# Optimization experiments

Measured on AMD Instinct MI355X. Metric: run time of the kernel, lower is better.

The kernel has to match this reference:

```python
import jax, jax.numpy as jnp
import numpy as np

NEG_SLOPE = 0.2  # PyG GATConv default leaky_relu slope


def gat_conv(x, src, dst, n, W, a_src, a_dst, bias, concat):
    """PyG-style GATConv (add_self_loops already applied to src/dst)."""
    H, C = a_src.shape
    h = (x @ W).reshape(n, H, C)                      # [N,H,C]
    al_src = jnp.einsum('nhc,hc->nh', h, a_src)       # [N,H]
    al_dst = jnp.einsum('nhc,hc->nh', h, a_dst)       # [N,H]
    e = jax.nn.leaky_relu(al_src[src] + al_dst[dst], NEG_SLOPE)  # [E,H]
    # segment softmax over incoming edges of each dst node
    m = jax.ops.segment_max(e, dst, num_segments=n)   # [N,H]
    ex = jnp.exp(e - m[dst])
    denom = jax.ops.segment_sum(ex, dst, num_segments=n)
    alpha = ex / denom[dst]                            # [E,H]
    out = jax.ops.segment_sum(h[src] * alpha[:, :, None], dst, num_segments=n)  # [N,H,C]
    if concat:
        out = out.reshape(n, H * C)
    else:
        out = out.mean(axis=1)
    return out + bias


def setup_inputs() -> dict:
    key = jax.random.key(0)
    ks = jax.random.split(key, 12)
    N, E = 100000, 1600000
    IN, HID, OUT, H = 128, 16, 32, 4
    x = jax.random.normal(ks[0], (N, IN), dtype=jnp.float32)
    edge_index = jax.random.randint(ks[1], (2, E), 0, N, dtype=jnp.int64)
    s = 0.1
    W1 = jax.random.normal(ks[2], (IN, H * HID), dtype=jnp.float32) * s
    a_src1 = jax.random.normal(ks[3], (H, HID), dtype=jnp.float32) * s
    a_dst1 = jax.random.normal(ks[4], (H, HID), dtype=jnp.float32) * s
    b1 = jnp.zeros((H * HID,), dtype=jnp.float32)
    W2 = jax.random.normal(ks[5], (H * HID, H * OUT), dtype=jnp.float32) * s
    a_src2 = jax.random.normal(ks[6], (H, OUT), dtype=jnp.float32) * s
    a_dst2 = jax.random.normal(ks[7], (H, OUT), dtype=jnp.float32) * s
    b2 = jnp.zeros((OUT,), dtype=jnp.float32)
    return {"x": x, "edge_index": edge_index,
            "W1": W1, "a_src1": a_src1, "a_dst1": a_dst1, "b1": b1,
            "W2": W2, "a_src2": a_src2, "a_dst2": a_dst2, "b2": b2}


def reference(x, edge_index, W1, a_src1, a_dst1, b1, W2, a_src2, a_dst2, b2):
    n = x.shape[0]
    loop = jnp.arange(n, dtype=edge_index.dtype)
    src = jnp.concatenate([edge_index[0], loop])
    dst = jnp.concatenate([edge_index[1], loop])
    # dropout is identity at inference
    h = gat_conv(x, src, dst, n, W1, a_src1, a_dst1, b1, concat=True)
    h = gat_conv(h, src, dst, n, W2, a_src2, a_dst2, b2, concat=False)
    h = jax.nn.elu(h)
    return jax.nn.log_softmax(h, axis=1)
```

## Files before the change

### kernel.cpp

```cpp
#include <hip/hip_runtime.h>
#include <hip/hip_fp16.h>
#include <cstdint>
#include <cstddef>

#define NEG 0.2f
#define TILE 4096
#define WEXP(e) __expf((e) > 0.f ? (e) : NEG * (e))

typedef int i4v __attribute__((ext_vector_type(4)));

__device__ __forceinline__ i4v ld_i4(const int* p) {
    i4v r;
    __builtin_memcpy(&r, p, 16);
    return r;
}
__device__ __forceinline__ __half2 bch(unsigned v) { __half2 r; *(unsigned*)&r = v; return r; }
__device__ __forceinline__ __half2 bchi(int v) { __half2 r; *(int*)&r = v; return r; }


__global__ __launch_bounds__(256) void bhist_k(const int* __restrict__ ei, int* __restrict__ bc, int E, int nbk) {
    __shared__ int sb[256];
    int t = threadIdx.x;
    sb[t] = 0;
    __syncthreads();
    int stride = gridDim.x * 256;
    for (int i = blockIdx.x * 256 + t; i < E; i += stride) {
        int d = __builtin_nontemporal_load(ei + E + i);
        atomicAdd(&sb[d >> 9], 1);
    }
    __syncthreads();
    if (t < nbk && sb[t] > 0) atomicAdd(&bc[t], sb[t]);
}


__global__ __launch_bounds__(256) void bscan_k(const int* __restrict__ bc, int* __restrict__ bb,
                                               int* __restrict__ curA, int nbk) {
    __shared__ int sm[256];
    int t = threadIdx.x;
    int v = (t < nbk) ? bc[t] : 0;
    sm[t] = v; __syncthreads();
    for (int off = 1; off < 256; off <<= 1) {
        int u = (t >= off) ? sm[t - off] : 0;
        __syncthreads();
        sm[t] += u;
        __syncthreads();
    }
    if (t < nbk) {
        int ex = sm[t] - v;
        bb[t] = ex;
        curA[t] = ex;
        if (t == nbk - 1) bb[nbk] = sm[t];
    }
}


__global__ __launch_bounds__(256) void partA_k(const int* __restrict__ ei, int* __restrict__ curA,
                                               uint2* __restrict__ pairs, int E, int nbk) {
    __shared__ int scnt[256];
    __shared__ int sc[256];
    __shared__ int sbase[256];
    __shared__ int gbase[256];
    __shared__ int cur2[256];
    __shared__ int ssrc[TILE];
    __shared__ int sdst[TILE];
    int t = threadIdx.x;
    int ntiles = (E + TILE - 1) / TILE;
    for (int tile = blockIdx.x; tile < ntiles; tile += gridDim.x) {
        int base = tile * TILE;
        int cntE = min(TILE, E - base);
        scnt[t] = 0;
        __syncthreads();
        int mys[16], myd[16];
        #pragma unroll
        for (int j = 0; j < 16; j++) {
            int i = base + t + 256 * j;
            int s = 0, d = -1;
            if (i < E) {
                s = __builtin_nontemporal_load(ei + i);
                d = __builtin_nontemporal_load(ei + E + i);
            }
            mys[j] = s; myd[j] = d;
            if (d >= 0) atomicAdd(&scnt[d >> 9], 1);
        }
        __syncthreads();
        sc[t] = scnt[t];
        __syncthreads();
        for (int off = 1; off < 256; off <<= 1) {
            int u = (t >= off) ? sc[t - off] : 0;
            __syncthreads();
            sc[t] += u;
            __syncthreads();
        }
        int myb = sc[t] - scnt[t];
        sbase[t] = myb;
        cur2[t] = myb;
        if (t < nbk && scnt[t] > 0) gbase[t] = atomicAdd(&curA[t], scnt[t]);
        __syncthreads();
        #pragma unroll
        for (int j = 0; j < 16; j++) {
            int d = myd[j];
            if (d >= 0) {
                int b = d >> 9;
                int pos = atomicAdd(&cur2[b], 1);
                ssrc[pos] = mys[j];
                sdst[pos] = d;
            }
        }
        __syncthreads();
        for (int i = t; i < cntE; i += 256) {
            int d = sdst[i];
            int b = d >> 9;
            int addr = gbase[b] + (i - sbase[b]);
            pairs[addr] = make_uint2((unsigned)ssrc[i], (unsigned)d);
        }
        __syncthreads();
    }
}


__global__ __launch_bounds__(256) void partB2_k(const uint2* __restrict__ pin, const int* __restrict__ bb,
                                                int* __restrict__ rp, int* __restrict__ cnt,
                                                int* __restrict__ srcout, int N) {
    __shared__ int cur[512];
    __shared__ int sc[512];
    int b = blockIdx.x, t = threadIdx.x;
    int d0 = b << 9;
    cur[t] = 0; cur[t + 256] = 0;
    __syncthreads();
    int ebase = bb[b], eend = bb[b + 1];
    for (int j = ebase + t; j < eend; j += 256) {
        int d = (int)pin[j].y;
        atomicAdd(&cur[d - d0], 1);
    }
    __syncthreads();
    sc[t] = cur[t]; sc[t + 256] = cur[t + 256];
    __syncthreads();
    for (int off = 1; off <= 256; off <<= 1) {
        int a0 = (t >= off) ? sc[t - off] : 0;
        int a1 = sc[t + 256 - off];
        __syncthreads();
        sc[t] += a0; sc[t + 256] += a1;
        __syncthreads();
    }
    int base0 = ebase + sc[t] - cur[t];
    int base1 = ebase + sc[t + 256] - cur[t + 256];
    if (d0 + t < N)       { rp[d0 + t] = base0;       cnt[d0 + t] = cur[t]; }
    if (d0 + t + 256 < N) { rp[d0 + t + 256] = base1; cnt[d0 + t + 256] = cur[t + 256]; }
    cur[t] = base0; cur[t + 256] = base1;
    __syncthreads();
    for (int j = ebase + t; j < eend; j += 256) {
        uint2 p = pin[j];
        int d = (int)p.y;
        int pos = rp[d] + 0;
        pos = atomicAdd(&cur[d - d0], 1);
        srcout[pos] = (int)p.x;
    }
}


__global__ __launch_bounds__(256) void gemm1_k(const float* __restrict__ x, const float* __restrict__ W,
                                               const float* __restrict__ a_src, const float* __restrict__ a_dst,
                                               __half* __restrict__ h, float* __restrict__ alsrc,
                                               float* __restrict__ aldst, int N) {
    __shared__ float Bs[128 * 64];
    __shared__ float xt[64 * 68];
    int t = threadIdx.x;
    for (int i = t; i < 128 * 64 / 4; i += 256)
        ((float4*)Bs)[i] = ((const float4*)W)[i];
    int ct = t & 15, rt = t >> 4;
    int head = ct >> 2, cq = ct & 3;
    float asv[4], adv[4];
    #pragma unroll
    for (int j = 0; j < 4; j++) {
        asv[j] = a_src[head * 16 + 4 * cq + j];
        adv[j] = a_dst[head * 16 + 4 * cq + j];
    }
    int ntiles = (N + 63) >> 6;
    for (int tile = blockIdx.x; tile < ntiles; tile += gridDim.x) {
        int r0 = tile << 6;
        float acc[4][4];
        #pragma unroll
        for (int i = 0; i < 4; i++)
            #pragma unroll
            for (int j = 0; j < 4; j++) acc[i][j] = 0.f;
        for (int kc = 0; kc < 128; kc += 64) {
            __syncthreads();
            int srow = t >> 4, sf4 = t & 15;
            #pragma unroll
            for (int p = 0; p < 4; p++) {
                int r = r0 + srow + 16 * p;
                float4 v = make_float4(0.f, 0.f, 0.f, 0.f);
                if (r < N) v = *(const float4*)(x + (size_t)r * 128 + kc + 4 * sf4);
                int rr = srow + 16 * p, k0 = 4 * sf4;
                int colb = 4 * (((rr >> 2) + sf4) & 15) + (rr & 3);
                xt[(k0 + 0) * 68 + colb] = v.x;
                xt[(k0 + 1) * 68 + colb] = v.y;
                xt[(k0 + 2) * 68 + colb] = v.z;
                xt[(k0 + 3) * 68 + colb] = v.w;
            }
            __syncthreads();
            #pragma unroll 4
            for (int k = 0; k < 64; k++) {
                float4 bv = *(float4*)&Bs[(kc + k) * 64 + 4 * ct];
                float4 xv = *(float4*)&xt[k * 68 + 4 * ((rt + (k >> 2)) & 15)];
                acc[0][0] = fmaf(xv.x, bv.x, acc[0][0]);
                acc[0][1] = fmaf(xv.x, bv.y, acc[0][1]);
                acc[0][2] = fmaf(xv.x, bv.z, acc[0][2]);
                acc[0][3] = fmaf(xv.x, bv.w, acc[0][3]);
                acc[1][0] = fmaf(xv.y, bv.x, acc[1][0]);
                acc[1][1] = fmaf(xv.y, bv.y, acc[1][1]);
                acc[1][2] = fmaf(xv.y, bv.z, acc[1][2]);
                acc[1][3] = fmaf(xv.y, bv.w, acc[1][3]);
                acc[2][0] = fmaf(xv.z, bv.x, acc[2][0]);
                acc[2][1] = fmaf(xv.z, bv.y, acc[2][1]);
                acc[2][2] = fmaf(xv.z, bv.z, acc[2][2]);
                acc[2][3] = fmaf(xv.z, bv.w, acc[2][3]);
                acc[3][0] = fmaf(xv.w, bv.x, acc[3][0]);
                acc[3][1] = fmaf(xv.w, bv.y, acc[3][1]);
                acc[3][2] = fmaf(xv.w, bv.z, acc[3][2]);
                acc[3][3] = fmaf(xv.w, bv.w, acc[3][3]);
            }
        }
        #pragma unroll
        for (int i = 0; i < 4; i++) {
            int r = r0 + 4 * rt + i;
            float ps = 0.f, pd = 0.f;
            #pragma unroll
            for (int j = 0; j < 4; j++) {
                ps = fmaf(acc[i][j], asv[j], ps);
                pd = fmaf(acc[i][j], adv[j], pd);
            }
            ps += __shfl_xor(ps, 1); ps += __shfl_xor(ps, 2);
            pd += __shfl_xor(pd, 1); pd += __shfl_xor(pd, 2);
            if (r < N) {
                __half2 h0 = __floats2half2_rn(acc[i][0], acc[i][1]);
                __half2 h1 = __floats2half2_rn(acc[i][2], acc[i][3]);
                *(__half2*)(h + (size_t)r * 64 + 4 * ct) = h0;
                *(__half2*)(h + (size_t)r * 64 + 4 * ct + 2) = h1;
                if (cq == 0) { alsrc[r * 4 + head] = ps; aldst[r * 4 + head] = pd; }
            }
        }
    }
}


__global__ __launch_bounds__(256) void prew_k(const float* __restrict__ W2, const float* __restrict__ as2,
                                              const float* __restrict__ ad2, float* __restrict__ was,
                                              float* __restrict__ wad, unsigned* __restrict__ wkh) {
    int t = threadIdx.x;
    int k = t >> 2, hh = t & 3;
    const float* wrow = W2 + k * 128 + hh * 32;
    const float* av = as2 + hh * 32;
    const float* dv = ad2 + hh * 32;
    float s = 0.f, ds = 0.f;
    #pragma unroll 8
    for (int c = 0; c < 32; c++) {
        float w = wrow[c];
        s = fmaf(w, av[c], s);
        ds = fmaf(w, dv[c], ds);
    }
    was[t] = s;
    wad[t] = ds;
    #pragma unroll
    for (int j = 0; j < 16; j++) {
        int e = t * 16 + j;
        int r = e >> 6, cc = e & 63;
        int col = cc >> 1, par = cc & 1;
        int p = 2 * r + par;
        int h = p >> 5, kk = (2 * p) & 63;
        float f0 = W2[kk * 128 + h * 32 + col];
        float f1 = W2[(kk + 1) * 128 + h * 32 + col];
        __half2 hv = __floats2half2_rn(f0, f1);
        wkh[e] = *(unsigned*)&hv;
    }
}


__global__ __launch_bounds__(256) void node1_k(const __half* __restrict__ h, const int* __restrict__ srccol,
                                               const float* __restrict__ alsrc, const float* __restrict__ aldst,
                                               const int* __restrict__ rp, const int* __restrict__ cnt,
                                               const float* __restrict__ bias,
                                               const float* __restrict__ was, const float* __restrict__ wad,
                                               __half* __restrict__ out,
                                               float* __restrict__ alsrc2, float* __restrict__ aldst2, int N) {
    int t = threadIdx.x;
    int d = (blockIdx.x * 256 + t) >> 4;
    if (d >= N) return;
    int c = t & 15;
    int eh = c >> 2, hh = c & 3;
    int mh = c >> 2;
    const uint2* hb = (const uint2*)h;
    float myad = aldst[d * 4 + hh];
    float selfw = WEXP(alsrc[d * 4 + hh] + myad);
    __half2 sh2 = __float2half2_rn(selfw);
    int si = *(int*)&sh2;
    float mden = (eh == 0) ? selfw : 0.f;
    uint2 u = hb[((size_t)d << 4) + c];
    __half2 smy = bchi(__shfl(si, mh, 16));
    __half2 acc0 = __hmul2(smy, bch(u.x));
    __half2 acc1 = __hmul2(smy, bch(u.y));
    int start = rp[d], deg = cnt[d];
    int nq = deg >> 2;
    int i = 0;
    #define N1_PROC(G0, G1, G2, G3, AW) { \
        float w_ = WEXP((AW) + myad); \
        mden += w_; \
        __half2 wh_ = __float2half2_rn(w_); \
        int wi_ = *(int*)&wh_; \
        __half2 q0_ = bchi(__shfl(wi_, 0 + mh, 16)); \
        __half2 q1_ = bchi(__shfl(wi_, 4 + mh, 16)); \
        __half2 q2_ = bchi(__shfl(wi_, 8 + mh, 16)); \
        __half2 q3_ = bchi(__shfl(wi_, 12 + mh, 16)); \
        acc0 = __hfma2(q0_, bch(G0.x), acc0); acc1 = __hfma2(q0_, bch(G0.y), acc1); \
        acc0 = __hfma2(q1_, bch(G1.x), acc0); acc1 = __hfma2(q1_, bch(G1.y), acc1); \
        acc0 = __hfma2(q2_, bch(G2.x), acc0); acc1 = __hfma2(q2_, bch(G2.y), acc1); \
        acc0 = __hfma2(q3_, bch(G3.x), acc0); acc1 = __hfma2(q3_, bch(G3.y), acc1); }
    if (nq > 0) {
        i4v sv = ld_i4(srccol + start);
        uint2 g0 = hb[((size_t)(unsigned)sv.x << 4) + c];
        uint2 g1 = hb[((size_t)(unsigned)sv.y << 4) + c];
        uint2 g2 = hb[((size_t)(unsigned)sv.z << 4) + c];
        uint2 g3 = hb[((size_t)(unsigned)sv.w << 4) + c];
        int my = (eh == 0) ? sv.x : (eh == 1) ? sv.y : (eh == 2) ? sv.z : sv.w;
        float aw = alsrc[(size_t)my * 4 + hh];
        i4v nv = (nq > 1) ? ld_i4(srccol + start + 4) : sv;
        for (int q = 1; q < nq; q++) {
            uint2 n0 = hb[((size_t)(unsigned)nv.x << 4) + c];
            uint2 n1 = hb[((size_t)(unsigned)nv.y << 4) + c];
            uint2 n2 = hb[((size_t)(unsigned)nv.z << 4) + c];
            uint2 n3 = hb[((size_t)(unsigned)nv.w << 4) + c];
            int nmy = (eh == 0) ? nv.x : (eh == 1) ? nv.y : (eh == 2) ? nv.z : nv.w;
            float naw = alsrc[(size_t)nmy * 4 + hh];
            i4v nv2 = (q + 1 < nq) ? ld_i4(srccol + start + 4 * (q + 1)) : nv;
            N1_PROC(g0, g1, g2, g3, aw)
            g0 = n0; g1 = n1; g2 = n2; g3 = n3; aw = naw; nv = nv2;
        }
        N1_PROC(g0, g1, g2, g3, aw)
        i = nq << 2;
    }
    for (; i < deg; i++) {
        int s = srccol[start + i];
        uint2 us = hb[((size_t)(unsigned)s << 4) + c];
        float w = WEXP(alsrc[(size_t)s * 4 + hh] + myad);
        mden += (eh == 0) ? w : 0.f;
        __half2 wh = __float2half2_rn(w);
        int wi = *(int*)&wh;
        __half2 qq = bchi(__shfl(wi, mh, 16));
        acc0 = __hfma2(qq, bch(us.x), acc0);
        acc1 = __hfma2(qq, bch(us.y), acc1);
    }
    mden += __shfl_xor(mden, 4, 16);
    mden += __shfl_xor(mden, 8, 16);
    float den = __shfl(mden, mh, 16);
    float inv = 1.f / den;
    float2 f0 = __half22float2(acc0), f1 = __half22float2(acc1);
    float4 b = *(const float4*)(bias + 4 * c);
    float v0 = f0.x * inv + b.x, v1 = f0.y * inv + b.y;
    float v2 = f1.x * inv + b.z, v3 = f1.y * inv + b.w;
    __half2 o0 = __floats2half2_rn(v0, v1);
    __half2 o1 = __floats2half2_rn(v2, v3);
    uint2 o; o.x = *(unsigned*)&o0; o.y = *(unsigned*)&o1;
    *(uint2*)(out + (size_t)d * 64 + 4 * c) = o;
    const float4* was4 = (const float4*)was;
    const float4* wad4 = (const float4*)wad;
    float4 wa0 = was4[4 * c + 0], wa1 = was4[4 * c + 1], wa2 = was4[4 * c + 2], wa3 = was4[4 * c + 3];
    float4 wd0 = wad4[4 * c + 0], wd1 = wad4[4 * c + 1], wd2 = wad4[4 * c + 2], wd3 = wad4[4 * c + 3];
    float4 ps, pd;
    ps.x = fmaf(v0, wa0.x, fmaf(v1, wa1.x, fmaf(v2, wa2.x, v3 * wa3.x)));
    ps.y = fmaf(v0, wa0.y, fmaf(v1, wa1.y, fmaf(v2, wa2.y, v3 * wa3.y)));
    ps.z = fmaf(v0, wa0.z, fmaf(v1, wa1.z, fmaf(v2, wa2.z, v3 * wa3.z)));
    ps.w = fmaf(v0, wa0.w, fmaf(v1, wa1.w, fmaf(v2, wa2.w, v3 * wa3.w)));
    pd.x = fmaf(v0, wd0.x, fmaf(v1, wd1.x, fmaf(v2, wd2.x, v3 * wd3.x)));
    pd.y = fmaf(v0, wd0.y, fmaf(v1, wd1.y, fmaf(v2, wd2.y, v3 * wd3.y)));
    pd.z = fmaf(v0, wd0.z, fmaf(v1, wd1.z, fmaf(v2, wd2.z, v3 * wd3.z)));
    pd.w = fmaf(v0, wd0.w, fmaf(v1, wd1.w, fmaf(v2, wd2.w, v3 * wd3.w)));
    #pragma unroll
    for (int off = 1; off <= 8; off <<= 1) {
        ps.x += __shfl_xor(ps.x, off); ps.y += __shfl_xor(ps.y, off);
        ps.z += __shfl_xor(ps.z, off); ps.w += __shfl_xor(ps.w, off);
        pd.x += __shfl_xor(pd.x, off); pd.y += __shfl_xor(pd.y, off);
        pd.z += __shfl_xor(pd.z, off); pd.w += __shfl_xor(pd.w, off);
    }
    if (c == 0) {
        *(float4*)(alsrc2 + (size_t)d * 4) = ps;
        *(float4*)(aldst2 + (size_t)d * 4) = pd;
    }
}


#define EDGE_SH(J, U) { \
    __half2 l_ = bch(U.x), h_ = bch(U.y); \
    __half2 qa = bchi(__shfl(wi, 4 * J + 0, 16)); \
    __half2 qb = bchi(__shfl(wi, 4 * J + 1, 16)); \
    __half2 qc = bchi(__shfl(wi, 4 * J + 2, 16)); \
    __half2 qd = bchi(__shfl(wi, 4 * J + 3, 16)); \
    aA0 = __hfma2(qa, l_, aA0); aA1 = __hfma2(qa, h_, aA1); \
    aB0 = __hfma2(qb, l_, aB0); aB1 = __hfma2(qb, h_, aB1); \
    aC0 = __hfma2(qc, l_, aC0); aC1 = __hfma2(qc, h_, aC1); \
    aD0 = __hfma2(qd, l_, aD0); aD1 = __hfma2(qd, h_, aD1); }

__global__ __launch_bounds__(256) void node2_k(const __half* __restrict__ h1o, const int* __restrict__ srccol,
                                               const float* __restrict__ alsrc, const float* __restrict__ aldst,
                                               const int* __restrict__ rp, const int* __restrict__ cnt,
                                               const unsigned* __restrict__ wkh, const float* __restrict__ b2,
                                               float* __restrict__ out, int N) {
    __shared__ unsigned wkl[64 * 68];
    int t = threadIdx.x;
    #pragma unroll
    for (int j = 0; j < 16; j++) {
        int g = t * 16 + j;
        wkl[(g >> 6) * 68 + (g & 63)] = wkh[g];
    }
    __syncthreads();
    int d = (blockIdx.x * 256 + t) >> 4;
    if (d >= N) return;
    int c = t & 15;
    int eh = c >> 2;
    int hh = c & 3;
    const uint2* hb = (const uint2*)h1o;
    float myad = aldst[d * 4 + hh];
    float selfw = WEXP(alsrc[d * 4 + hh] + myad);
    __half2 selfh = __float2half2_rn(selfw);
    int selfi = *(int*)&selfh;
    float mden = (eh == 0) ? selfw : 0.f;
    uint2 u = hb[((size_t)d << 4) + c];
    __half2 lo = bch(u.x), hi = bch(u.y);
    __half2 sA = bchi(__shfl(selfi, 0, 16));
    __half2 sB = bchi(__shfl(selfi, 1, 16));
    __half2 sC = bchi(__shfl(selfi, 2, 16));
    __half2 sD = bchi(__shfl(selfi, 3, 16));
    __half2 aA0 = __hmul2(sA, lo), aA1 = __hmul2(sA, hi);
    __half2 aB0 = __hmul2(sB, lo), aB1 = __hmul2(sB, hi);
    __half2 aC0 = __hmul2(sC, lo), aC1 = __hmul2(sC, hi);
    __half2 aD0 = __hmul2(sD, lo), aD1 = __hmul2(sD, hi);
    int start = rp[d], deg = cnt[d];
    int nq = deg >> 2;
    int i = 0;
    #define N2_PROC(G0, G1, G2, G3, AW) { \
        float w_ = WEXP((AW) + myad); \
        mden += w_; \
        __half2 wh_ = __float2half2_rn(w_); \
        int wi = *(int*)&wh_; \
        EDGE_SH(0, G0) EDGE_SH(1, G1) EDGE_SH(2, G2) EDGE_SH(3, G3) }
    if (nq > 0) {
        i4v sv = ld_i4(srccol + start);
        uint2 g0 = hb[((size_t)(unsigned)sv.x << 4) + c];
        uint2 g1 = hb[((size_t)(unsigned)sv.y << 4) + c];
        uint2 g2 = hb[((size_t)(unsigned)sv.z << 4) + c];
        uint2 g3 = hb[((size_t)(unsigned)sv.w << 4) + c];
        int my = (eh == 0) ? sv.x : (eh == 1) ? sv.y : (eh == 2) ? sv.z : sv.w;
        float aw = alsrc[(size_t)my * 4 + hh];
        i4v nv = (nq > 1) ? ld_i4(srccol + start + 4) : sv;
        for (int q = 1; q < nq; q++) {
            uint2 n0 = hb[((size_t)(unsigned)nv.x << 4) + c];
            uint2 n1 = hb[((size_t)(unsigned)nv.y << 4) + c];
            uint2 n2 = hb[((size_t)(unsigned)nv.z << 4) + c];
            uint2 n3 = hb[((size_t)(unsigned)nv.w << 4) + c];
            int nmy = (eh == 0) ? nv.x : (eh == 1) ? nv.y : (eh == 2) ? nv.z : nv.w;
            float naw = alsrc[(size_t)nmy * 4 + hh];
            i4v nv2 = (q + 1 < nq) ? ld_i4(srccol + start + 4 * (q + 1)) : nv;
            N2_PROC(g0, g1, g2, g3, aw)
            g0 = n0; g1 = n1; g2 = n2; g3 = n3; aw = naw; nv = nv2;
        }
        N2_PROC(g0, g1, g2, g3, aw)
        i = nq << 2;
    }
    for (; i < deg; i++) {
        int s = srccol[start + i];
        uint2 us = hb[((size_t)(unsigned)s << 4) + c];
        float w = WEXP(alsrc[(size_t)s * 4 + hh] + myad);
        mden += (eh == 0) ? w : 0.f;
        __half2 wh = __float2half2_rn(w);
        int wi = *(int*)&wh;
        EDGE_SH(0, us)
    }
    mden += __shfl_xor(mden, 4, 16);
    mden += __shfl_xor(mden, 8, 16);
    float dnA = __shfl(mden, 0, 16);
    float dnB = __shfl(mden, 1, 16);
    float dnC = __shfl(mden, 2, 16);
    float dnD = __shfl(mden, 3, 16);
    __half2 jA = __float2half2_rn(0.25f / dnA), jB = __float2half2_rn(0.25f / dnB);
    __half2 jC = __float2half2_rn(0.25f / dnC), jD = __float2half2_rn(0.25f / dnD);
    __half2 y00 = __hmul2(jA, aA0), y01 = __hmul2(jA, aA1);
    __half2 y10 = __hmul2(jB, aB0), y11 = __hmul2(jB, aB1);
    __half2 y20 = __hmul2(jC, aC0), y21 = __hmul2(jC, aC1);
    __half2 y30 = __hmul2(jD, aD0), y31 = __hmul2(jD, aD1);
    __half2 acc[32];
    __half2 hz = __float2half2_rn(0.f);
    #pragma unroll
    for (int j = 0; j < 32; j++) acc[j] = hz;
    #define EPI_H(H, P0, P1) { \
        const unsigned* wr = wkl + (16 * H + c) * 68; \
        _Pragma("unroll") \
        for (int i2 = 0; i2 < 16; i2++) { \
            uint4 w = *(const uint4*)&wr[4 * i2]; \
            acc[2 * i2]     = __hfma2(P0, bch(w.x), acc[2 * i2]); \
            acc[2 * i2]     = __hfma2(P1, bch(w.y), acc[2 * i2]); \
            acc[2 * i2 + 1] = __hfma2(P0, bch(w.z), acc[2 * i2 + 1]); \
            acc[2 * i2 + 1] = __hfma2(P1, bch(w.w), acc[2 * i2 + 1]); \
        } }
    EPI_H(0, y00, y01)
    EPI_H(1, y10, y11)
    EPI_H(2, y20, y21)
    EPI_H(3, y30, y31)
    float o[32];
    #pragma unroll
    for (int j = 0; j < 32; j++) {
        float2 f = __half22float2(acc[j]);
        o[j] = f.x + f.y;
    }
    #pragma unroll
    for (int off = 1; off <= 8; off <<= 1) {
        #pragma unroll
        for (int j = 0; j < 32; j++) o[j] += __shfl_xor(o[j], off, 16);
    }
    #pragma unroll
    for (int j = 0; j < 32; j++) {
        float e = o[j] + b2[j];
        o[j] = e > 0.f ? e : __expf(e) - 1.f;
    }
    float mx = o[0];
    #pragma unroll
    for (int j = 1; j < 32; j++) mx = fmaxf(mx, o[j]);
    float sm = 0.f;
    #pragma unroll
    for (int j = 0; j < 32; j++) sm += __expf(o[j] - mx);
    float ls = mx + __logf(sm);
    float* op = out + (size_t)d * 32;
    #pragma unroll
    for (int g = 0; g < 8; g++) {
        if (c == g) {
            float4 v;
            v.x = o[4 * g + 0] - ls;
            v.y = o[4 * g + 1] - ls;
            v.z = o[4 * g + 2] - ls;
            v.w = o[4 * g + 3] - ls;
            *(float4*)(op + 4 * g) = v;
        }
    }
}


extern "C" void kernel_launch(void* const* d_in, const int* in_sizes, int n_in,
                              void* d_out, int out_size, void* d_ws, size_t ws_size,
                              hipStream_t stream) {
    const float* x   = (const float*)d_in[0];
    const int*   ei  = (const int*)d_in[1];
    const float* W1  = (const float*)d_in[2];
    const float* as1 = (const float*)d_in[3];
    const float* ad1 = (const float*)d_in[4];
    const float* b1  = (const float*)d_in[5];
    const float* W2  = (const float*)d_in[6];
    const float* as2 = (const float*)d_in[7];
    const float* ad2 = (const float*)d_in[8];
    const float* b2  = (const float*)d_in[9];
    float* out = (float*)d_out;
    int N = in_sizes[0] / 128;
    int E = in_sizes[1] / 2;

    char* base = (char*)d_ws;
    size_t off = 0;
    auto alloc = [&](size_t bytes) -> char* {
        char* p = base + off;
        off = (off + bytes + 255) & ~(size_t)255;
        return p;
    };
    __half* h1h   = (__half*)alloc((size_t)N * 64 * 2);
    __half* h1o   = (__half*)alloc((size_t)N * 64 * 2);
    uint2*  pairs = (uint2*)alloc((size_t)E * 8);
    float* alsrc1 = (float*)alloc((size_t)N * 4 * 4);
    float* aldst1 = (float*)alloc((size_t)N * 4 * 4);
    float* alsrc2 = (float*)alloc((size_t)N * 4 * 4);
    float* aldst2 = (float*)alloc((size_t)N * 4 * 4);
    float* was    = (float*)alloc(256 * 4);
    float* wad    = (float*)alloc(256 * 4);
    unsigned* wkh = (unsigned*)alloc(4096 * 4);
    int* cnt  = (int*)alloc((size_t)N * 4);
    int* rp   = (int*)alloc((size_t)N * 4);
    int* curA = (int*)alloc(256 * 4);
    int* bc   = (int*)alloc(256 * 4);
    int* bb   = (int*)alloc(260 * 4);
    int* srccol = (int*)alloc((size_t)E * 4);

    int nbk = (N + 511) >> 9;
    int ntilesA = (E + TILE - 1) / TILE;
    int nt1 = (N + 63) >> 6;

    prew_k<<<1, 256, 0, stream>>>(W2, as2, ad2, was, wad, wkh);
    hipMemsetAsync(bc, 0, 256 * 4, stream);
    bhist_k<<<512, 256, 0, stream>>>(ei, bc, E, nbk);
    bscan_k<<<1, 256, 0, stream>>>(bc, bb, curA, nbk);
    partA_k<<<ntilesA, 256, 0, stream>>>(ei, curA, pairs, E, nbk);
    partB2_k<<<nbk, 256, 0, stream>>>(pairs, bb, rp, cnt, srccol, N);

    gemm1_k<<<(nt1 + 1) / 2, 256, 0, stream>>>(x, W1, as1, ad1, h1h, alsrc1, aldst1, N);
    node1_k<<<(N + 15) / 16, 256, 0, stream>>>(h1h, srccol, alsrc1, aldst1, rp, cnt, b1,
                                               was, wad, h1o, alsrc2, aldst2, N);
    node2_k<<<(N + 15) / 16, 256, 0, stream>>>(h1o, srccol, alsrc2, aldst2, rp, cnt,
                                               wkh, b2, out, N);
}
```

Baseline: 331.2 us.

## Restructure node2 epilogue as shared-memory tile matmul with per-lane output columns

The layer-2 projection epilogue in node2_k is reorganized. Each lane used to compute all 32 outputs from its own slice and then needed a 32-wide butterfly reduction. Now the aggregated per-node vectors are staged in shared memory, and each lane computes two output columns over the full 128-wide K dimension from a transposed weight tile. This removes the 32x4 shuffle reductions and per-lane 32-element softmax work, at the cost of an extra block barrier and more LDS traffic. A dead rp load in the partition kernel is also removed.

```diff
diff --git a/kernel.cpp b/kernel.cpp
--- a/kernel.cpp
+++ b/kernel.cpp
@@ -151,8 +151,7 @@
     for (int j = ebase + t; j < eend; j += 256) {
         uint2 p = pin[j];
         int d = (int)p.y;
-        int pos = rp[d] + 0;
-        pos = atomicAdd(&cur[d - d0], 1);
+        int pos = atomicAdd(&cur[d - d0], 1);
         srcout[pos] = (int)p.x;
     }
 }
@@ -246,7 +245,7 @@
 
 __global__ __launch_bounds__(256) void prew_k(const float* __restrict__ W2, const float* __restrict__ as2,
                                               const float* __restrict__ ad2, float* __restrict__ was,
-                                              float* __restrict__ wad, unsigned* __restrict__ wkh) {
+                                              float* __restrict__ wad, uint2* __restrict__ wkg) {
     int t = threadIdx.x;
     int k = t >> 2, hh = t & 3;
     const float* wrow = W2 + k * 128 + hh * 32;
@@ -262,16 +261,18 @@
     was[t] = s;
     wad[t] = ds;
     #pragma unroll
-    for (int j = 0; j < 16; j++) {
-        int e = t * 16 + j;
-        int r = e >> 6, cc = e & 63;
-        int col = cc >> 1, par = cc & 1;
-        int p = 2 * r + par;
-        int h = p >> 5, kk = (2 * p) & 63;
-        float f0 = W2[kk * 128 + h * 32 + col];
-        float f1 = W2[(kk + 1) * 128 + h * 32 + col];
-        __half2 hv = __floats2half2_rn(f0, f1);
-        wkh[e] = *(unsigned*)&hv;
+    for (int j = 0; j < 8; j++) {
+        int e = t * 8 + j;
+        int cp = e >> 7, k2 = e & 127;
+        int h = k2 >> 5, kk = (2 * k2) & 63;
+        const float* w0 = W2 + kk * 128 + h * 32;
+        const float* w1 = W2 + (kk + 1) * 128 + h * 32;
+        __half2 hx = __floats2half2_rn(w0[2 * cp], w1[2 * cp]);
+        __half2 hy = __floats2half2_rn(w0[2 * cp + 1], w1[2 * cp + 1]);
+        uint2 v;
+        v.x = *(unsigned*)&hx;
+        v.y = *(unsigned*)&hy;
+        wkg[e] = v;
     }
 }
 
@@ -402,143 +403,137 @@
 __global__ __launch_bounds__(256) void node2_k(const __half* __restrict__ h1o, const int* __restrict__ srccol,
                                                const float* __restrict__ alsrc, const float* __restrict__ aldst,
                                                const int* __restrict__ rp, const int* __restrict__ cnt,
-                                               const unsigned* __restrict__ wkh, const float* __restrict__ b2,
+                                               const uint2* __restrict__ wkg, const float* __restrict__ b2,
                                                float* __restrict__ out, int N) {
-    __shared__ unsigned wkl[64 * 68];
+    __shared__ unsigned wt[16 * 260];
+    __shared__ unsigned ys[16 * 132];
     int t = threadIdx.x;
     #pragma unroll
-    for (int j = 0; j < 16; j++) {
-        int g = t * 16 + j;
-        wkl[(g >> 6) * 68 + (g & 63)] = wkh[g];
-    }
-    __syncthreads();
-    int d = (blockIdx.x * 256 + t) >> 4;
-    if (d >= N) return;
+    for (int j = 0; j < 8; j++) {
+        int i = t + 256 * j;
+        int cp0 = i >> 7, k20 = i & 127;
+        *(uint2*)&wt[cp0 * 260 + 2 * k20] = wkg[i];
+    }
+    int d = blockIdx.x * 16 + (t >> 4);
     int c = t & 15;
-    int eh = c >> 2;
-    int hh = c & 3;
-    const uint2* hb = (const uint2*)h1o;
-    float myad = aldst[d * 4 + hh];
-    float selfw = WEXP(alsrc[d * 4 + hh] + myad);
-    __half2 selfh = __float2half2_rn(selfw);
-    int selfi = *(int*)&selfh;
-    float mden = (eh == 0) ? selfw : 0.f;
-    uint2 u = hb[((size_t)d << 4) + c];
-    __half2 lo = bch(u.x), hi = bch(u.y);
-    __half2 sA = bchi(__shfl(selfi, 0, 16));
-    __half2 sB = bchi(__shfl(selfi, 1, 16));
-    __half2 sC = bchi(__shfl(selfi, 2, 16));
-    __half2 sD = bchi(__shfl(selfi, 3, 16));
-    __half2 aA0 = __hmul2(sA, lo), aA1 = __hmul2(sA, hi);
-    __half2 aB0 = __hmul2(sB, lo), aB1 = __hmul2(sB, hi);
-    __half2 aC0 = __hmul2(sC, lo), aC1 = __hmul2(sC, hi);
-    __half2 aD0 = __hmul2(sD, lo), aD1 = __hmul2(sD, hi);
-    int start = rp[d], deg = cnt[d];
-    int nq = deg >> 2;
-    int i = 0;
-    #define N2_PROC(G0, G1, G2, G3, AW) { \
-        float w_ = WEXP((AW) + myad); \
-        mden += w_; \
-        __half2 wh_ = __float2half2_rn(w_); \
-        int wi = *(int*)&wh_; \
-        EDGE_SH(0, G0) EDGE_SH(1, G1) EDGE_SH(2, G2) EDGE_SH(3, G3) }
-    if (nq > 0) {
-        i4v sv = ld_i4(srccol + start);
-        uint2 g0 = hb[((size_t)(unsigned)sv.x << 4) + c];
-        uint2 g1 = hb[((size_t)(unsigned)sv.y << 4) + c];
-        uint2 g2 = hb[((size_t)(unsigned)sv.z << 4) + c];
-        uint2 g3 = hb[((size_t)(unsigned)sv.w << 4) + c];
-        int my = (eh == 0) ? sv.x : (eh == 1) ? sv.y : (eh == 2) ? sv.z : sv.w;
-        float aw = alsrc[(size_t)my * 4 + hh];
-        i4v nv = (nq > 1) ? ld_i4(srccol + start + 4) : sv;
-        for (int q = 1; q < nq; q++) {
-            uint2 n0 = hb[((size_t)(unsigned)nv.x << 4) + c];
-            uint2 n1 = hb[((size_t)(unsigned)nv.y << 4) + c];
-            uint2 n2 = hb[((size_t)(unsigned)nv.z << 4) + c];
-            uint2 n3 = hb[((size_t)(unsigned)nv.w << 4) + c];
-            int nmy = (eh == 0) ? nv.x : (eh == 1) ? nv.y : (eh == 2) ? nv.z : nv.w;
-            float naw = alsrc[(size_t)nmy * 4 + hh];
-            i4v nv2 = (q + 1 < nq) ? ld_i4(srccol + start + 4 * (q + 1)) : nv;
+    bool live = d < N;
+    __half2 hz = __float2half2_rn(0.f);
+    __half2 y00 = hz, y01 = hz, y10 = hz, y11 = hz;
+    __half2 y20 = hz, y21 = hz, y30 = hz, y31 = hz;
+    if (live) {
+        int eh = c >> 2;
+        int hh = c & 3;
+        const uint2* hb = (const uint2*)h1o;
+        float myad = aldst[d * 4 + hh];
+        float selfw = WEXP(alsrc[d * 4 + hh] + myad);
+        __half2 selfh = __float2half2_rn(selfw);
+        int selfi = *(int*)&selfh;
+        float mden = (eh == 0) ? selfw : 0.f;
+        uint2 u = hb[((size_t)d << 4) + c];
+        __half2 lo = bch(u.x), hi = bch(u.y);
+        __half2 sA = bchi(__shfl(selfi, 0, 16));
+        __half2 sB = bchi(__shfl(selfi, 1, 16));
+        __half2 sC = bchi(__shfl(selfi, 2, 16));
+        __half2 sD = bchi(__shfl(selfi, 3, 16));
+        __half2 aA0 = __hmul2(sA, lo), aA1 = __hmul2(sA, hi);
+        __half2 aB0 = __hmul2(sB, lo), aB1 = __hmul2(sB, hi);
+        __half2 aC0 = __hmul2(sC, lo), aC1 = __hmul2(sC, hi);
+        __half2 aD0 = __hmul2(sD, lo), aD1 = __hmul2(sD, hi);
+        int start = rp[d], deg = cnt[d];
+        int nq = deg >> 2;
+        int i = 0;
+        #define N2_PROC(G0, G1, G2, G3, AW) { \
+            float w_ = WEXP((AW) + myad); \
+            mden += w_; \
+            __half2 wh_ = __float2half2_rn(w_); \
+            int wi = *(int*)&wh_; \
+            EDGE_SH(0, G0) EDGE_SH(1, G1) EDGE_SH(2, G2) EDGE_SH(3, G3) }
+        if (nq > 0) {
+            i4v sv = ld_i4(srccol + start);
+            uint2 g0 = hb[((size_t)(unsigned)sv.x << 4) + c];
+            uint2 g1 = hb[((size_t)(unsigned)sv.y << 4) + c];
+            uint2 g2 = hb[((size_t)(unsigned)sv.z << 4) + c];
+            uint2 g3 = hb[((size_t)(unsigned)sv.w << 4) + c];
+            int my = (eh == 0) ? sv.x : (eh == 1) ? sv.y : (eh == 2) ? sv.z : sv.w;
+            float aw = alsrc[(size_t)my * 4 + hh];
+            i4v nv = (nq > 1) ? ld_i4(srccol + start + 4) : sv;
+            for (int q = 1; q < nq; q++) {
+                uint2 n0 = hb[((size_t)(unsigned)nv.x << 4) + c];
+                uint2 n1 = hb[((size_t)(unsigned)nv.y << 4) + c];
+                uint2 n2 = hb[((size_t)(unsigned)nv.z << 4) + c];
+                uint2 n3 = hb[((size_t)(unsigned)nv.w << 4) + c];
+                int nmy = (eh == 0) ? nv.x : (eh == 1) ? nv.y : (eh == 2) ? nv.z : nv.w;
+                float naw = alsrc[(size_t)nmy * 4 + hh];
+                i4v nv2 = (q + 1 < nq) ? ld_i4(srccol + start + 4 * (q + 1)) : nv;
+                N2_PROC(g0, g1, g2, g3, aw)
+                g0 = n0; g1 = n1; g2 = n2; g3 = n3; aw = naw; nv = nv2;
+            }
             N2_PROC(g0, g1, g2, g3, aw)
-            g0 = n0; g1 = n1; g2 = n2; g3 = n3; aw = naw; nv = nv2;
-        }
-        N2_PROC(g0, g1, g2, g3, aw)
-        i = nq << 2;
-    }
-    for (; i < deg; i++) {
-        int s = srccol[start + i];
-        uint2 us = hb[((size_t)(unsigned)s << 4) + c];
-        float w = WEXP(alsrc[(size_t)s * 4 + hh] + myad);
-        mden += (eh == 0) ? w : 0.f;
-        __half2 wh = __float2half2_rn(w);
-        int wi = *(int*)&wh;
-        EDGE_SH(0, us)
-    }
-    mden += __shfl_xor(mden, 4, 16);
-    mden += __shfl_xor(mden, 8, 16);
-    float dnA = __shfl(mden, 0, 16);
-    float dnB = __shfl(mden, 1, 16);
-    float dnC = __shfl(mden, 2, 16);
-    float dnD = __shfl(mden, 3, 16);
-    __half2 jA = __float2half2_rn(0.25f / dnA), jB = __float2half2_rn(0.25f / dnB);
-    __half2 jC = __float2half2_rn(0.25f / dnC), jD = __float2half2_rn(0.25f / dnD);
-    __half2 y00 = __hmul2(jA, aA0), y01 = __hmul2(jA, aA1);
-    __half2 y10 = __hmul2(jB, aB0), y11 = __hmul2(jB, aB1);
-    __half2 y20 = __hmul2(jC, aC0), y21 = __hmul2(jC, aC1);
-    __half2 y30 = __hmul2(jD, aD0), y31 = __hmul2(jD, aD1);
-    __half2 acc[32];
-    __half2 hz = __float2half2_rn(0.f);
+            i = nq << 2;
+        }
+        for (; i < deg; i++) {
+            int s = srccol[start + i];
+            uint2 us = hb[((size_t)(unsigned)s << 4) + c];
+            float w = WEXP(alsrc[(size_t)s * 4 + hh] + myad);
+            mden += (eh == 0) ? w : 0.f;
+            __half2 wh = __float2half2_rn(w);
+            int wi = *(int*)&wh;
+            EDGE_SH(0, us)
+        }
+        mden += __shfl_xor(mden, 4, 16);
+        mden += __shfl_xor(mden, 8, 16);
+        float dnA = __shfl(mden, 0, 16);
+        float dnB = __shfl(mden, 1, 16);
+        float dnC = __shfl(mden, 2, 16);
+        float dnD = __shfl(mden, 3, 16);
+        __half2 jA = __float2half2_rn(0.25f / dnA), jB = __float2half2_rn(0.25f / dnB);
+        __half2 jC = __float2half2_rn(0.25f / dnC), jD = __float2half2_rn(0.25f / dnD);
+        y00 = __hmul2(jA, aA0); y01 = __hmul2(jA, aA1);
+        y10 = __hmul2(jB, aB0); y11 = __hmul2(jB, aB1);
+        y20 = __hmul2(jC, aC0); y21 = __hmul2(jC, aC1);
+        y30 = __hmul2(jD, aD0); y31 = __hmul2(jD, aD1);
+        unsigned* yp = ys + (t >> 4) * 132 + 2 * c;
+        *(uint2*)&yp[0]  = make_uint2(*(unsigned*)&y00, *(unsigned*)&y01);
+        *(uint2*)&yp[32] = make_uint2(*(unsigned*)&y10, *(unsigned*)&y11);
+        *(uint2*)&yp[64] = make_uint2(*(unsigned*)&y20, *(unsigned*)&y21);
+        *(uint2*)&yp[96] = make_uint2(*(unsigned*)&y30, *(unsigned*)&y31);
+    }
+    __syncthreads();
+    if (!live) return;
+    int n = t >> 4, cp = c;
+    const unsigned* yr = ys + n * 132;
+    const unsigned* wr = wt + cp * 260;
+    float f0 = 0.f, f1 = 0.f;
+    for (int kc = 0; kc < 128; kc += 16) {
+        __half2 a0 = hz, a1 = hz;
+        #pragma unroll
+        for (int j = 0; j < 4; j++) {
+            int k2 = kc + 4 * j;
+            uint4 yv = *(const uint4*)&yr[k2];
+            uint4 w0 = *(const uint4*)&wr[2 * k2];
+            uint4 w1 = *(const uint4*)&wr[2 * k2 + 4];
+            a0 = __hfma2(bch(yv.x), bch(w0.x), a0); a1 = __hfma2(bch(yv.x), bch(w0.y), a1);
+            a0 = __hfma2(bch(yv.y), bch(w0.z), a0); a1 = __hfma2(bch(yv.y), bch(w0.w), a1);
+            a0 = __hfma2(bch(yv.z), bch(w1.x), a0); a1 = __hfma2(bch(yv.z), bch(w1.y), a1);
+            a0 = __hfma2(bch(yv.w), bch(w1.z), a0); a1 = __hfma2(bch(yv.w), bch(w1.w), a1);
+        }
+        float2 q0 = __half22float2(a0), q1 = __half22float2(a1);
+        f0 += q0.x + q0.y;
+        f1 += q1.x + q1.y;
+    }
+    float e0 = f0 + b2[2 * cp];
+    float e1 = f1 + b2[2 * cp + 1];
+    e0 = e0 > 0.f ? e0 : __expf(e0) - 1.f;
+    e1 = e1 > 0.f ? e1 : __expf(e1) - 1.f;
+    float mx = fmaxf(e0, e1);
     #pragma unroll
-    for (int j = 0; j < 32; j++) acc[j] = hz;
-    #define EPI_H(H, P0, P1) { \
-        const unsigned* wr = wkl + (16 * H + c) * 68; \
-        _Pragma("unroll") \
-        for (int i2 = 0; i2 < 16; i2++) { \
-            uint4 w = *(const uint4*)&wr[4 * i2]; \
-            acc[2 * i2]     = __hfma2(P0, bch(w.x), acc[2 * i2]); \
-            acc[2 * i2]     = __hfma2(P1, bch(w.y), acc[2 * i2]); \
-            acc[2 * i2 + 1] = __hfma2(P0, bch(w.z), acc[2 * i2 + 1]); \
-            acc[2 * i2 + 1] = __hfma2(P1, bch(w.w), acc[2 * i2 + 1]); \
-        } }
-    EPI_H(0, y00, y01)
-    EPI_H(1, y10, y11)
-    EPI_H(2, y20, y21)
-    EPI_H(3, y30, y31)
-    float o[32];
+    for (int off = 1; off <= 8; off <<= 1) mx = fmaxf(mx, __shfl_xor(mx, off, 16));
+    float sm = __expf(e0 - mx) + __expf(e1 - mx);
     #pragma unroll
-    for (int j = 0; j < 32; j++) {
-        float2 f = __half22float2(acc[j]);
-        o[j] = f.x + f.y;
-    }
-    #pragma unroll
-    for (int off = 1; off <= 8; off <<= 1) {
-        #pragma unroll
-        for (int j = 0; j < 32; j++) o[j] += __shfl_xor(o[j], off, 16);
-    }
-    #pragma unroll
-    for (int j = 0; j < 32; j++) {
-        float e = o[j] + b2[j];
-        o[j] = e > 0.f ? e : __expf(e) - 1.f;
-    }
-    float mx = o[0];
-    #pragma unroll
-    for (int j = 1; j < 32; j++) mx = fmaxf(mx, o[j]);
-    float sm = 0.f;
-    #pragma unroll
-    for (int j = 0; j < 32; j++) sm += __expf(o[j] - mx);
+    for (int off = 1; off <= 8; off <<= 1) sm += __shfl_xor(sm, off, 16);
     float ls = mx + __logf(sm);
-    float* op = out + (size_t)d * 32;
-    #pragma unroll
-    for (int g = 0; g < 8; g++) {
-        if (c == g) {
-            float4 v;
-            v.x = o[4 * g + 0] - ls;
-            v.y = o[4 * g + 1] - ls;
-            v.z = o[4 * g + 2] - ls;
-            v.w = o[4 * g + 3] - ls;
-            *(float4*)(op + 4 * g) = v;
-        }
-    }
+    float2 ov = make_float2(e0 - ls, e1 - ls);
+    *(float2*)(out + (size_t)d * 32 + 2 * cp) = ov;
 }
 
 
@@ -575,7 +570,7 @@
     float* aldst2 = (float*)alloc((size_t)N * 4 * 4);
     float* was    = (float*)alloc(256 * 4);
     float* wad    = (float*)alloc(256 * 4);
-    unsigned* wkh = (unsigned*)alloc(4096 * 4);
+    uint2* wkg    = (uint2*)alloc(2048 * 8);
     int* cnt  = (int*)alloc((size_t)N * 4);
     int* rp   = (int*)alloc((size_t)N * 4);
     int* curA = (int*)alloc(256 * 4);
@@ -587,7 +582,7 @@
     int ntilesA = (E + TILE - 1) / TILE;
     int nt1 = (N + 63) >> 6;
 
-    prew_k<<<1, 256, 0, stream>>>(W2, as2, ad2, was, wad, wkh);
+    prew_k<<<1, 256, 0, stream>>>(W2, as2, ad2, was, wad, wkg);
     hipMemsetAsync(bc, 0, 256 * 4, stream);
     bhist_k<<<512, 256, 0, stream>>>(ei, bc, E, nbk);
     bscan_k<<<1, 256, 0, stream>>>(bc, bb, curA, nbk);
@@ -598,5 +593,5 @@
     node1_k<<<(N + 15) / 16, 256, 0, stream>>>(h1h, srccol, alsrc1, aldst1, rp, cnt, b1,
                                                was, wad, h1o, alsrc2, aldst2, N);
     node2_k<<<(N + 15) / 16, 256, 0, stream>>>(h1o, srccol, alsrc2, aldst2, rp, cnt,
-                                               wkh, b2, out, N);
-}
+                                               wkg, b2, out, N);
+}
```

Measured after the change: 312.3 us. 1.06x faster.
